# Performance work log

Measured on AMD Instinct MI355X. Metric: run time of the kernel, lower is better.

## Reference

```python
import jax, jax.numpy as jnp
import numpy as np

N, D = 100000, 128

def _seg_softmax(vals, ids, n):
    # torch scatter_reduce amax with include_self=True over zeros init => max(0, seg max);
    # softmax is shift-invariant so this matches torch exactly and stays stable.
    m = jnp.maximum(jax.ops.segment_max(vals, ids, num_segments=n), 0.0)
    e = jnp.exp(vals - m[ids])
    s = jax.ops.segment_sum(e, ids, num_segments=n)
    return e / (s[ids] + 1e-9)

def setup_inputs() -> dict:
    key = jax.random.key(0)
    ks = jax.random.split(key, 24)
    d = D
    def lin(k, fi, fo):
        b = 1.0 / np.sqrt(fi)
        kw, kb = jax.random.split(k)
        return (jax.random.uniform(kw, (fi, fo), jnp.float32, -b, b),
                jax.random.uniform(kb, (fo,), jnp.float32, -b, b))
    Wae, bae = lin(ks[0], 2 * d, d)
    w0w, w0b = lin(ks[1], d, 1)
    War, bar = lin(ks[2], 2 * d, d)
    w1w, w1b = lin(ks[3], d, 1)
    W1, b1 = lin(ks[4], d, d)
    W2, b2 = lin(ks[5], d, d)
    W3, b3 = lin(ks[6], d, d)
    return {
        'node_emb': jax.random.normal(ks[7], (N, d), jnp.float32),
        'Wae': Wae, 'bae': bae, 'w0w': w0w[:, 0], 'w0b': w0b,
        'War': War, 'bar': bar, 'w1w': w1w[:, 0], 'w1b': w1b,
        'W1': W1, 'b1': b1, 'W2': W2, 'b2': b2, 'W3': W3, 'b3': b3,
        'er_src': jax.random.randint(ks[8], (500000,), 0, N),
        'er_dst': jax.random.randint(ks[9], (500000,), 0, N),
        'ee_src': jax.random.randint(ks[10], (500000,), 0, N),
        'ee_dst': jax.random.randint(ks[11], (500000,), 0, N),
        'rr_src': jax.random.randint(ks[12], (200000,), 0, N),
        'rr_dst': jax.random.randint(ks[13], (200000,), 0, N),
    }

def reference(node_emb, Wae, bae, w0w, w0b, War, bar, w1w, w1b,
              W1, b1, W2, b2, W3, b3,
              er_src, er_dst, ee_src, ee_dst, rr_src, rr_dst):
    n = node_emb.shape[0]
    h = node_emb[er_src]              # (E, d) head entity emb
    r = node_emb[er_dst]              # (E, d) relation emb
    # entity-side attention over relation neighbours
    pair_e = jnp.concatenate([r, h], axis=-1)
    e_ij = jnp.tanh(pair_e @ Wae + bae) @ w0w + w0b[0]
    attn_e = _seg_softmax(e_ij, er_src, n)
    attn_agg = jax.ops.segment_sum(attn_e[:, None] * r, er_src, num_segments=n)
    # relation-side attention over entity neighbours (separate params)
    pair_r = jnp.concatenate([h, r], axis=-1)
    e_ij_r = jnp.tanh(pair_r @ War + bar) @ w1w + w1b[0]
    attn_r = _seg_softmax(e_ij_r, er_dst, n)
    attn_agg = attn_agg + jax.ops.segment_sum(attn_r[:, None] * h, er_dst, num_segments=n)
    # unweighted mean over similar-entity and similar-relation edges
    mean_agg = jax.ops.segment_sum(node_emb[ee_dst], ee_src, num_segments=n)
    mean_agg = mean_agg + jax.ops.segment_sum(node_emb[rr_dst], rr_src, num_segments=n)
    cnt = jax.ops.segment_sum(jnp.ones(ee_src.shape[0], node_emb.dtype), ee_src, num_segments=n)
    cnt = cnt + jax.ops.segment_sum(jnp.ones(rr_src.shape[0], node_emb.dtype), rr_src, num_segments=n)
    mean_agg = mean_agg / jnp.maximum(cnt, 1.0)[:, None]
    return (jnp.tanh(node_emb @ W1 + b1)
            + jnp.tanh(attn_agg @ W2 + b2)
            + jnp.tanh(mean_agg @ W3 + b3))
```

## Files before the change

### kernel.cpp

```cpp
#include <hip/hip_runtime.h>
#include <hip/hip_bf16.h>

#define D 128
#define TILE 2048

typedef __bf16 bf16x8 __attribute__((ext_vector_type(8)));
typedef float f32x4 __attribute__((ext_vector_type(4)));
typedef unsigned short u16x8 __attribute__((ext_vector_type(8)));

__device__ __forceinline__ float tanh_fast(float x) {
    float e = __expf(2.0f * fabsf(x));
    float t = 1.0f - 2.0f * __builtin_amdgcn_rcpf(e + 1.0f);
    return copysignf(t, x);
}

__device__ __forceinline__ float bf2f(unsigned short u) {
    return __uint_as_float((unsigned int)u << 16);
}

__device__ __forceinline__ unsigned short f2bf_u16(float x) {
    __hip_bfloat16 t = __float2bfloat16(x);
    return *(unsigned short*)&t;
}

#define SWZ_F(x, imm) __int_as_float(__builtin_amdgcn_ds_swizzle(__float_as_int(x), imm))

__global__ __launch_bounds__(256) void detect_kernel(const unsigned short* __restrict__ x,
                                                     int* __restrict__ flag) {
    int t = threadIdx.x;
    int cnt = 0;
    for (int i = t; i < 4096; i += 256) {
        unsigned e = (x[i] >> 7) & 0xFFu;
        if (e == 0xFFu || e >= 0x90u || (e >= 1u && e <= 0x6Eu)) cnt++;
    }
    __shared__ int sh[256];
    sh[t] = cnt;
    __syncthreads();
    for (int off = 128; off; off >>= 1) {
        if (t < off) sh[t] += sh[t + off];
        __syncthreads();
    }
    if (t == 0) flag[0] = (sh[0] > 800) ? 1 : 0;
}

struct ConvBatch {
    const void* src[14];
    __hip_bfloat16* dst[14];
    int n[14];
};

__global__ __launch_bounds__(256) void conv_weights_kernel(ConvBatch cb,
                                                           const int* __restrict__ flag) {
    int a = blockIdx.y;
    const void* s = cb.src[a];
    unsigned short* d = (unsigned short*)cb.dst[a];
    int n = cb.n[a];
    int f = flag[0];
    int i = (blockIdx.x * 256 + threadIdx.x) * 4;
    if (i >= n) return;
    if (i + 4 <= n) {
        ushort4 o;
        if (f) {
            float4 v = *(const float4*)((const float*)s + i);
            o.x = f2bf_u16(v.x); o.y = f2bf_u16(v.y);
            o.z = f2bf_u16(v.z); o.w = f2bf_u16(v.w);
        } else {
            o = *(const ushort4*)((const unsigned short*)s + i);
        }
        *(ushort4*)(d + i) = o;
    } else {
        for (int j = i; j < n; j++)
            d[j] = f ? f2bf_u16(((const float*)s)[j])
                     : ((const unsigned short*)s)[j];
    }
}

__global__ __launch_bounds__(256) void conv_x_kernel(const void* __restrict__ src,
                                                     __hip_bfloat16* __restrict__ dst,
                                                     int n, const int* __restrict__ flag) {
    int i = (blockIdx.x * 256 + threadIdx.x) * 4;
    if (i >= n) return;
    int f = flag[0];
    ushort4 o;
    if (f) {
        float4 v = *(const float4*)((const float*)src + i);
        o.x = f2bf_u16(v.x); o.y = f2bf_u16(v.y);
        o.z = f2bf_u16(v.z); o.w = f2bf_u16(v.w);
    } else {
        o = *(const ushort4*)((const unsigned short*)src + i);
    }
    *(ushort4*)((unsigned short*)dst + i) = o;
}

struct TransBatch {
    const void* base[7];
    int off[7];
    unsigned short* dst[7];
};

__global__ __launch_bounds__(256) void trans_kernel(TransBatch tb,
                                                    const int* __restrict__ flag) {
    int a = blockIdx.y;
    int f = flag[0];
    const float* sf = (const float*)tb.base[a] + tb.off[a];
    const unsigned short* sb = (const unsigned short*)tb.base[a] + tb.off[a];
    unsigned short* d = tb.dst[a];
    int idx = (blockIdx.x * 256 + threadIdx.x) * 4;
    int k = idx >> 7, c = idx & 127;
    unsigned short v[4];
    if (f) {
        float4 x = *(const float4*)(sf + idx);
        v[0] = f2bf_u16(x.x); v[1] = f2bf_u16(x.y);
        v[2] = f2bf_u16(x.z); v[3] = f2bf_u16(x.w);
    } else {
        ushort4 x = *(const ushort4*)(sb + idx);
        v[0] = x.x; v[1] = x.y; v[2] = x.z; v[3] = x.w;
    }
#pragma unroll
    for (int j = 0; j < 4; j++) d[(c + j) * 128 + k] = v[j];
}

__global__ __launch_bounds__(256) void zero_kernel(int* p, int n) {
    int i = blockIdx.x * 256 + threadIdx.x;
    if (i < n) p[i] = 0;
}

__global__ __launch_bounds__(256) void count_kernel(const int* __restrict__ keys, int E,
                                                    int* __restrict__ deg) {
    int i = blockIdx.x * 256 + threadIdx.x;
    if (i < E) atomicAdd(&deg[keys[i]], 1);
}

__global__ __launch_bounds__(256) void scan_partial_kernel(const int* __restrict__ deg,
                                                           int* __restrict__ tsum,
                                                           int N, int ntpa) {
    int a = blockIdx.x / ntpa, t = blockIdx.x % ntpa;
    const int* d = deg + (size_t)a * N + (size_t)t * TILE;
    int lim = N - t * TILE; if (lim > TILE) lim = TILE;
    int base = threadIdx.x * 8;
    int s = 0;
#pragma unroll
    for (int j = 0; j < 8; j++) {
        int i = base + j;
        if (i < lim) s += d[i];
    }
    __shared__ int sh[256];
    sh[threadIdx.x] = s;
    __syncthreads();
    for (int off = 128; off; off >>= 1) {
        if (threadIdx.x < off) sh[threadIdx.x] += sh[threadIdx.x + off];
        __syncthreads();
    }
    if (threadIdx.x == 0) tsum[blockIdx.x] = sh[0];
}

__global__ __launch_bounds__(256) void scan_tiles_kernel(const int* __restrict__ tsum,
                                                         int* __restrict__ toff,
                                                         int* __restrict__ indptr,
                                                         int N, int ntpa) {
    __shared__ int tmp[256];
    int t = threadIdx.x;
    for (int a = 0; a < 4; a++) {
        int v = (t < ntpa) ? tsum[a * ntpa + t] : 0;
        tmp[t] = v;
        __syncthreads();
        for (int off = 1; off < 256; off <<= 1) {
            int u = (t >= off) ? tmp[t - off] : 0;
            __syncthreads();
            tmp[t] += u;
            __syncthreads();
        }
        if (t < ntpa) toff[a * ntpa + t] = tmp[t] - v;
        if (t == ntpa - 1) indptr[(size_t)a * (N + 1) + N] = tmp[t];
        __syncthreads();
    }
}

__global__ __launch_bounds__(256) void scan_final_kernel(int* __restrict__ degcur,
                                                         const int* __restrict__ toff,
                                                         int* __restrict__ indptr,
                                                         int N, int ntpa) {
    int a = blockIdx.x / ntpa, t = blockIdx.x % ntpa;
    int* d = degcur + (size_t)a * N + (size_t)t * TILE;
    int* ip = indptr + (size_t)a * (N + 1) + (size_t)t * TILE;
    int lim = N - t * TILE; if (lim > TILE) lim = TILE;
    int base = threadIdx.x * 8;
    int v[8];
    int s = 0;
#pragma unroll
    for (int j = 0; j < 8; j++) {
        int i = base + j;
        v[j] = (i < lim) ? d[i] : 0;
        s += v[j];
    }
    __shared__ int tmp[256];
    tmp[threadIdx.x] = s;
    __syncthreads();
    for (int off = 1; off < 256; off <<= 1) {
        int u = (threadIdx.x >= off) ? tmp[threadIdx.x - off] : 0;
        __syncthreads();
        tmp[threadIdx.x] += u;
        __syncthreads();
    }
    int run = toff[blockIdx.x] + tmp[threadIdx.x] - s;
#pragma unroll
    for (int j = 0; j < 8; j++) {
        int i = base + j;
        if (i < lim) { ip[i] = run; d[i] = run; run += v[j]; }
    }
}

__global__ __launch_bounds__(256) void scatter_attn_kernel(const int* __restrict__ keys,
                                                           const int* __restrict__ oths, int E,
                                                           int* __restrict__ cursor,
                                                           int* __restrict__ key_sorted,
                                                           int* __restrict__ oth_sorted) {
    int i = blockIdx.x * 256 + threadIdx.x;
    if (i < E) {
        int k = keys[i];
        int p = atomicAdd(&cursor[k], 1);
        key_sorted[p] = k;
        oth_sorted[p] = oths[i];
    }
}

__global__ __launch_bounds__(256) void scatter_mean_kernel(const int* __restrict__ keys,
                                                           const int* __restrict__ dsts, int E,
                                                           int* __restrict__ cursor,
                                                           int* __restrict__ dst_sorted) {
    int i = blockIdx.x * 256 + threadIdx.x;
    if (i < E) {
        int p = atomicAdd(&cursor[keys[i]], 1);
        dst_sorted[p] = dsts[i];
    }
}

__global__ __launch_bounds__(256) void gemm2_mfma_kernel(
    const __hip_bfloat16* __restrict__ X,
    const unsigned short* __restrict__ Wt,
    const __hip_bfloat16* __restrict__ bias,
    __hip_bfloat16* __restrict__ part0,
    __hip_bfloat16* __restrict__ part1, int N) {
    __shared__ __align__(16) unsigned short As[64 * 136];
    __shared__ __align__(16) unsigned short Bs[128 * 136];
    int n0 = blockIdx.x * 64;
    for (int idx = threadIdx.x; idx < 64 * 16; idx += 256) {
        int r = idx >> 4, ch = idx & 15;
        uint4 v = make_uint4(0u, 0u, 0u, 0u);
        int n = n0 + r;
        if (n < N) v = ((const uint4*)(X + (size_t)n * D))[ch];
        *(uint4*)&As[r * 136 + ch * 8] = v;
    }
    int w = threadIdx.x >> 6, lane = threadIdx.x & 63;
    int n15 = lane & 15, quad = lane >> 4;
    bf16x8 af[4];
    for (int half = 0; half < 2; half++) {
        for (int idx = threadIdx.x; idx < 128 * 16; idx += 256) {
            int r = idx >> 4, ch = idx & 15;
            uint4 v = ((const uint4*)(Wt + (size_t)(half * 128 + r) * D))[ch];
            *(uint4*)&Bs[r * 136 + ch * 8] = v;
        }
        __syncthreads();
        if (half == 0) {
            const unsigned short* arow = &As[(w * 16 + n15) * 136 + quad * 8];
#pragma unroll
            for (int t = 0; t < 4; t++) af[t] = *(const bf16x8*)(arow + t * 32);
        }
        __hip_bfloat16* outp = half ? part1 : part0;
        for (int c = 0; c < 8; c++) {
            f32x4 acc = {0.f, 0.f, 0.f, 0.f};
            const unsigned short* brow = &Bs[(c * 16 + n15) * 136 + quad * 8];
#pragma unroll
            for (int t = 0; t < 4; t++)
                acc = __builtin_amdgcn_mfma_f32_16x16x32_bf16(
                    af[t], *(const bf16x8*)(brow + t * 32), acc, 0, 0, 0);
            int col = c * 16 + n15;
            float b = half ? __bfloat162float(bias[col]) : 0.f;
#pragma unroll
            for (int i = 0; i < 4; i++) {
                int row = n0 + w * 16 + quad * 4 + i;
                if (row < N) outp[(size_t)row * D + col] = __float2bfloat16(acc[i] + b);
            }
        }
        if (half == 0) __syncthreads();
    }
}

__global__ __launch_bounds__(256) void final_mfma_kernel(
    const __hip_bfloat16* __restrict__ X, const __hip_bfloat16* __restrict__ Agg,
    const __hip_bfloat16* __restrict__ Mn,
    const unsigned short* __restrict__ Wt1, const __hip_bfloat16* __restrict__ b1,
    const unsigned short* __restrict__ Wt2, const __hip_bfloat16* __restrict__ b2,
    const unsigned short* __restrict__ Wt3, const __hip_bfloat16* __restrict__ b3,
    void* __restrict__ out, const int* __restrict__ flag, int N) {
    __shared__ __align__(16) unsigned short As[64 * 136];
    __shared__ __align__(16) unsigned short Bs[128 * 136];
    int n0 = blockIdx.x * 64;
    int w = threadIdx.x >> 6, lane = threadIdx.x & 63;
    int n15 = lane & 15, quad = lane >> 4;
    float osum[8][4];
#pragma unroll
    for (int c = 0; c < 8; c++)
#pragma unroll
        for (int i = 0; i < 4; i++) osum[c][i] = 0.f;
    const __hip_bfloat16* srcs[3] = {X, Agg, Mn};
    const unsigned short* Wts[3] = {Wt1, Wt2, Wt3};
    const __hip_bfloat16* bs[3] = {b1, b2, b3};
    for (int m = 0; m < 3; m++) {
        if (m > 0) __syncthreads();
        const __hip_bfloat16* S = srcs[m];
        const unsigned short* Wm = Wts[m];
        for (int idx = threadIdx.x; idx < 64 * 16; idx += 256) {
            int r = idx >> 4, ch = idx & 15;
            uint4 v = make_uint4(0u, 0u, 0u, 0u);
            int n = n0 + r;
            if (n < N) v = ((const uint4*)(S + (size_t)n * D))[ch];
            *(uint4*)&As[r * 136 + ch * 8] = v;
        }
        for (int idx = threadIdx.x; idx < 128 * 16; idx += 256) {
            int r = idx >> 4, ch = idx & 15;
            uint4 v = ((const uint4*)(Wm + (size_t)r * D))[ch];
            *(uint4*)&Bs[r * 136 + ch * 8] = v;
        }
        __syncthreads();
        const unsigned short* arow = &As[(w * 16 + n15) * 136 + quad * 8];
        bf16x8 af[4];
#pragma unroll
        for (int t = 0; t < 4; t++) af[t] = *(const bf16x8*)(arow + t * 32);
        for (int c = 0; c < 8; c++) {
            f32x4 acc = {0.f, 0.f, 0.f, 0.f};
            const unsigned short* brow = &Bs[(c * 16 + n15) * 136 + quad * 8];
#pragma unroll
            for (int t = 0; t < 4; t++)
                acc = __builtin_amdgcn_mfma_f32_16x16x32_bf16(
                    af[t], *(const bf16x8*)(brow + t * 32), acc, 0, 0, 0);
            float bb = __bfloat162float(bs[m][c * 16 + n15]);
#pragma unroll
            for (int i = 0; i < 4; i++) osum[c][i] += tanh_fast(acc[i] + bb);
        }
    }
    int f = flag[0];
    for (int c = 0; c < 8; c++) {
        int col = c * 16 + n15;
#pragma unroll
        for (int i = 0; i < 4; i++) {
            int row = n0 + w * 16 + quad * 4 + i;
            if (row < N) {
                if (f) ((float*)out)[(size_t)row * D + col] = osum[c][i];
                else   ((__hip_bfloat16*)out)[(size_t)row * D + col] =
                           __float2bfloat16(osum[c][i]);
            }
        }
    }
}

__global__ __launch_bounds__(256) void edge_score_kernel(
    const __hip_bfloat16* __restrict__ Pkey,
    const __hip_bfloat16* __restrict__ Poth,
    const int* __restrict__ key_s,
    const int* __restrict__ oth_s,
    const __hip_bfloat16* __restrict__ w,
    const __hip_bfloat16* __restrict__ wb,
    float* __restrict__ eij, int E) {
    int l = threadIdx.x & 15;
    int gid = (int)((blockIdx.x * 256 + threadIdx.x) >> 4);
    int ngroups = (int)((gridDim.x * 256) >> 4);
    u16x8 wv = *(const u16x8*)((const unsigned short*)w + l * 8);
    float wf[8];
#pragma unroll
    for (int j = 0; j < 8; j++) wf[j] = bf2f(wv[j]);
    float wbv = bf2f(*(const unsigned short*)wb);
    const unsigned short* PK = (const unsigned short*)Pkey;
    const unsigned short* PO = (const unsigned short*)Poth;
    for (int s = gid; s < E; s += ngroups) {
        int key = key_s[s], oth = oth_s[s];
        u16x8 a = *(const u16x8*)(PK + (size_t)key * D + l * 8);
        u16x8 b = *(const u16x8*)(PO + (size_t)oth * D + l * 8);
        float p = 0.f;
#pragma unroll
        for (int j = 0; j < 8; j++)
            p = fmaf(tanh_fast(bf2f(a[j]) + bf2f(b[j])), wf[j], p);
        p += SWZ_F(p, 0x041F);
        p += SWZ_F(p, 0x081F);
        p += SWZ_F(p, 0x101F);
        p += SWZ_F(p, 0x201F);
        if (l == 0) eij[s] = p + wbv;
    }
}

__global__ __launch_bounds__(256) void attn_node_kernel(
    const __hip_bfloat16* __restrict__ X,
    const float* __restrict__ eij_e, const int* __restrict__ ip_e,
    const int* __restrict__ oth_e,
    const float* __restrict__ eij_r, const int* __restrict__ ip_r,
    const int* __restrict__ oth_r,
    __hip_bfloat16* __restrict__ attn_agg, int N) {
    int g = (int)((blockIdx.x * 256 + threadIdx.x) >> 4);
    int l = threadIdx.x & 15;
    if (g >= N) return;
    const unsigned short* Xp = (const unsigned short*)X;
    float acc[8];
#pragma unroll
    for (int j = 0; j < 8; j++) acc[j] = 0.f;
    for (int side = 0; side < 2; side++) {
        const float* eij = side ? eij_r : eij_e;
        const int* ip  = side ? ip_r  : ip_e;
        const int* oth = side ? oth_r : oth_e;
        int s0 = ip[g], s1 = ip[g + 1];
        if (s1 == s0) continue;
        float m = 0.f;
        for (int i = s0 + l; i < s1; i += 16) m = fmaxf(m, eij[i]);
        m = fmaxf(m, SWZ_F(m, 0x041F));
        m = fmaxf(m, SWZ_F(m, 0x081F));
        m = fmaxf(m, SWZ_F(m, 0x101F));
        m = fmaxf(m, SWZ_F(m, 0x201F));
        float ssum = 0.f;
        for (int i = s0 + l; i < s1; i += 16) ssum += __expf(eij[i] - m);
        ssum += SWZ_F(ssum, 0x041F);
        ssum += SWZ_F(ssum, 0x081F);
        ssum += SWZ_F(ssum, 0x101F);
        ssum += SWZ_F(ssum, 0x201F);
        float inv = 1.f / (ssum + 1e-9f);
        int i = s0;
        for (; i + 2 <= s1; i += 2) {
            int o0 = oth[i], o1 = oth[i + 1];
            u16x8 x0 = *(const u16x8*)(Xp + (size_t)o0 * D + l * 8);
            u16x8 x1 = *(const u16x8*)(Xp + (size_t)o1 * D + l * 8);
            float p0 = __expf(eij[i] - m) * inv;
            float p1 = __expf(eij[i + 1] - m) * inv;
#pragma unroll
            for (int j = 0; j < 8; j++)
                acc[j] += p0 * bf2f(x0[j]) + p1 * bf2f(x1[j]);
        }
        if (i < s1) {
            int o0 = oth[i];
            u16x8 x0 = *(const u16x8*)(Xp + (size_t)o0 * D + l * 8);
            float p0 = __expf(eij[i] - m) * inv;
#pragma unroll
            for (int j = 0; j < 8; j++) acc[j] += p0 * bf2f(x0[j]);
        }
    }
    u16x8 ov;
#pragma unroll
    for (int j = 0; j < 8; j++) ov[j] = f2bf_u16(acc[j]);
    *(u16x8*)((unsigned short*)attn_agg + (size_t)g * D + l * 8) = ov;
}

__global__ __launch_bounds__(256) void mean_node_kernel(
    const __hip_bfloat16* __restrict__ X,
    const int* __restrict__ ip_ee, const int* __restrict__ dst_ee,
    const int* __restrict__ ip_rr, const int* __restrict__ dst_rr,
    __hip_bfloat16* __restrict__ mean_agg, int N) {
    int g = (int)((blockIdx.x * 256 + threadIdx.x) >> 4);
    int l = threadIdx.x & 15;
    if (g >= N) return;
    const unsigned short* Xp = (const unsigned short*)X;
    float acc[8];
#pragma unroll
    for (int j = 0; j < 8; j++) acc[j] = 0.f;
    int cnt = 0;
    for (int side = 0; side < 2; side++) {
        const int* ip  = side ? ip_rr  : ip_ee;
        const int* dst = side ? dst_rr : dst_ee;
        int s0 = ip[g], s1 = ip[g + 1];
        cnt += s1 - s0;
        int i = s0;
        for (; i + 2 <= s1; i += 2) {
            int o0 = dst[i], o1 = dst[i + 1];
            u16x8 x0 = *(const u16x8*)(Xp + (size_t)o0 * D + l * 8);
            u16x8 x1 = *(const u16x8*)(Xp + (size_t)o1 * D + l * 8);
#pragma unroll
            for (int j = 0; j < 8; j++)
                acc[j] += bf2f(x0[j]) + bf2f(x1[j]);
        }
        if (i < s1) {
            u16x8 x0 = *(const u16x8*)(Xp + (size_t)dst[i] * D + l * 8);
#pragma unroll
            for (int j = 0; j < 8; j++) acc[j] += bf2f(x0[j]);
        }
    }
    float inv = 1.f / fmaxf((float)cnt, 1.f);
    u16x8 ov;
#pragma unroll
    for (int j = 0; j < 8; j++) ov[j] = f2bf_u16(acc[j] * inv);
    *(u16x8*)((unsigned short*)mean_agg + (size_t)g * D + l * 8) = ov;
}

extern "C" void kernel_launch(void* const* d_in, const int* in_sizes, int n_in,
                              void* d_out, int out_size, void* d_ws, size_t ws_size,
                              hipStream_t stream) {
    const int* er_src = (const int*)d_in[15];
    const int* er_dst = (const int*)d_in[16];
    const int* ee_src = (const int*)d_in[17];
    const int* ee_dst = (const int*)d_in[18];
    const int* rr_src = (const int*)d_in[19];
    const int* rr_dst = (const int*)d_in[20];

    int N   = in_sizes[0] / D;
    int Eer = in_sizes[15];
    int Eee = in_sizes[17];
    int Err = in_sizes[19];

    char* ws = (char*)d_ws;
    size_t off = 0;
    auto alloc = [&](size_t bytes) -> void* {
        void* p = ws + off;
        off = (off + bytes + 255) & ~(size_t)255;
        return p;
    };
    int ntpa = (N + TILE - 1) / TILE;
    int T = 4 * ntpa;
    int* flag   = (int*)alloc(256);
    int* key_se = (int*)alloc((size_t)Eer * 4);
    int* key_sr = (int*)alloc((size_t)Eer * 4);
    int* oth_e  = (int*)alloc((size_t)Eer * 4);
    int* oth_r  = (int*)alloc((size_t)Eer * 4);
    int* dst_ee = (int*)alloc((size_t)Eee * 4);
    int* dst_rr = (int*)alloc((size_t)Err * 4);
    int* indptr = (int*)alloc((size_t)4 * (N + 1) * 4);
    int* degcur = (int*)alloc((size_t)4 * N * 4);
    int* tsum   = (int*)alloc((size_t)T * 4);
    int* toff   = (int*)alloc((size_t)T * 4);
    float* eij_e = (float*)alloc((size_t)Eer * 4);
    float* eij_r = (float*)alloc((size_t)Eer * 4);
    __hip_bfloat16* Xc = (__hip_bfloat16*)alloc((size_t)N * D * 2);
    __hip_bfloat16* part0 = (__hip_bfloat16*)alloc((size_t)N * D * 2);
    __hip_bfloat16* part1 = (__hip_bfloat16*)alloc((size_t)N * D * 2);
    __hip_bfloat16* attn_agg = part0;
    __hip_bfloat16* mean_agg = part1;
    unsigned short* WtA = (unsigned short*)alloc((size_t)256 * 128 * 2);
    unsigned short* WtR = (unsigned short*)alloc((size_t)256 * 128 * 2);
    unsigned short* Wt1 = (unsigned short*)alloc((size_t)128 * 128 * 2);
    unsigned short* Wt2 = (unsigned short*)alloc((size_t)128 * 128 * 2);
    unsigned short* Wt3 = (unsigned short*)alloc((size_t)128 * 128 * 2);
    ConvBatch cb;
    int widx[14] = {1, 2, 3, 4, 5, 6, 7, 8, 9, 10, 11, 12, 13, 14};
    for (int i = 0; i < 14; i++) {
        cb.src[i] = d_in[widx[i]];
        cb.n[i] = in_sizes[widx[i]];
        cb.dst[i] = (__hip_bfloat16*)alloc((size_t)cb.n[i] * 2);
    }
    const __hip_bfloat16* bae = cb.dst[1];
    const __hip_bfloat16* w0w = cb.dst[2];
    const __hip_bfloat16* w0b = cb.dst[3];
    const __hip_bfloat16* bar_= cb.dst[5];
    const __hip_bfloat16* w1w = cb.dst[6];
    const __hip_bfloat16* w1b = cb.dst[7];
    const __hip_bfloat16* b1  = cb.dst[9];
    const __hip_bfloat16* b2  = cb.dst[11];
    const __hip_bfloat16* b3  = cb.dst[13];
    (void)n_in; (void)out_size;
    if (off > ws_size) return;

    detect_kernel<<<1, 256, 0, stream>>>((const unsigned short*)d_in[0], flag);
    conv_weights_kernel<<<dim3(32, 14), 256, 0, stream>>>(cb, flag);
    conv_x_kernel<<<(N * D / 4 + 255) / 256, 256, 0, stream>>>(d_in[0], Xc, N * D, flag);
    TransBatch tb;
    tb.base[0] = d_in[1];  tb.off[0] = 0;         tb.dst[0] = WtA;
    tb.base[1] = d_in[1];  tb.off[1] = 128 * 128; tb.dst[1] = WtA + 128 * 128;
    tb.base[2] = d_in[5];  tb.off[2] = 0;         tb.dst[2] = WtR;
    tb.base[3] = d_in[5];  tb.off[3] = 128 * 128; tb.dst[3] = WtR + 128 * 128;
    tb.base[4] = d_in[9];  tb.off[4] = 0;         tb.dst[4] = Wt1;
    tb.base[5] = d_in[11]; tb.off[5] = 0;         tb.dst[5] = Wt2;
    tb.base[6] = d_in[13]; tb.off[6] = 0;         tb.dst[6] = Wt3;
    trans_kernel<<<dim3(16, 7), 256, 0, stream>>>(tb, flag);

    zero_kernel<<<(4 * N + 255) / 256, 256, 0, stream>>>(degcur, 4 * N);
    count_kernel<<<(Eer + 255) / 256, 256, 0, stream>>>(er_src, Eer, degcur);
    count_kernel<<<(Eer + 255) / 256, 256, 0, stream>>>(er_dst, Eer, degcur + N);
    count_kernel<<<(Eee + 255) / 256, 256, 0, stream>>>(ee_src, Eee, degcur + 2 * N);
    count_kernel<<<(Err + 255) / 256, 256, 0, stream>>>(rr_src, Err, degcur + 3 * N);
    scan_partial_kernel<<<T, 256, 0, stream>>>(degcur, tsum, N, ntpa);
    scan_tiles_kernel<<<1, 256, 0, stream>>>(tsum, toff, indptr, N, ntpa);
    scan_final_kernel<<<T, 256, 0, stream>>>(degcur, toff, indptr, N, ntpa);
    scatter_attn_kernel<<<(Eer + 255) / 256, 256, 0, stream>>>(er_src, er_dst, Eer,
                                                               degcur, key_se, oth_e);
    scatter_attn_kernel<<<(Eer + 255) / 256, 256, 0, stream>>>(er_dst, er_src, Eer,
                                                               degcur + N, key_sr, oth_r);
    scatter_mean_kernel<<<(Eee + 255) / 256, 256, 0, stream>>>(ee_src, ee_dst, Eee,
                                                               degcur + 2 * N, dst_ee);
    scatter_mean_kernel<<<(Err + 255) / 256, 256, 0, stream>>>(rr_src, rr_dst, Err,
                                                               degcur + 3 * N, dst_rr);

    int GB = (N + 63) / 64;
    int EB = 2048;

    gemm2_mfma_kernel<<<GB, 256, 0, stream>>>(Xc, WtA, bae, part0, part1, N);
    edge_score_kernel<<<EB, 256, 0, stream>>>(part1, part0, key_se, oth_e,
                                              w0w, w0b, eij_e, Eer);

    gemm2_mfma_kernel<<<GB, 256, 0, stream>>>(Xc, WtR, bar_, part0, part1, N);
    edge_score_kernel<<<EB, 256, 0, stream>>>(part1, part0, key_sr, oth_r,
                                              w1w, w1b, eij_r, Eer);

    int NG = (N + 15) / 16;
    attn_node_kernel<<<NG, 256, 0, stream>>>(Xc, eij_e, indptr, oth_e,
                                             eij_r, indptr + (N + 1), oth_r,
                                             attn_agg, N);
    mean_node_kernel<<<NG, 256, 0, stream>>>(Xc, indptr + 2 * (N + 1), dst_ee,
                                             indptr + 3 * (N + 1), dst_rr,
                                             mean_agg, N);
    final_mfma_kernel<<<GB, 256, 0, stream>>>(Xc, attn_agg, mean_agg,
                                              Wt1, b1, Wt2, b2, Wt3, b3,
                                              d_out, flag, N);
}
```

Before: 583.8 us.

## Keep GEMM weights resident in LDS and load activations directly to registers

The gemm2 and final MFMA kernels now load all weight matrices into shared memory once per block. They then loop over row tiles in a grid-stride fashion, reading activation fragments straight from global memory into registers instead of staging them through LDS. Block sizes grow to 512 and 1024 threads, and the grids are capped at 2048 blocks. This removes the repeated weight reloads and per-tile barriers, but the larger LDS footprint (about 104 KB in the final kernel) can limit occupancy.

```diff
diff --git a/kernel.cpp b/kernel.cpp
--- a/kernel.cpp
+++ b/kernel.cpp
@@ -235,120 +235,126 @@
     }
 }
 
-__global__ __launch_bounds__(256) void gemm2_mfma_kernel(
+__global__ __launch_bounds__(512) void gemm2_mfma_kernel(
     const __hip_bfloat16* __restrict__ X,
     const unsigned short* __restrict__ Wt,
     const __hip_bfloat16* __restrict__ bias,
     __hip_bfloat16* __restrict__ part0,
     __hip_bfloat16* __restrict__ part1, int N) {
-    __shared__ __align__(16) unsigned short As[64 * 136];
-    __shared__ __align__(16) unsigned short Bs[128 * 136];
-    int n0 = blockIdx.x * 64;
-    for (int idx = threadIdx.x; idx < 64 * 16; idx += 256) {
+    __shared__ __align__(16) unsigned short Bs[256 * 136];
+    for (int idx = threadIdx.x; idx < 256 * 16; idx += 512) {
         int r = idx >> 4, ch = idx & 15;
-        uint4 v = make_uint4(0u, 0u, 0u, 0u);
-        int n = n0 + r;
-        if (n < N) v = ((const uint4*)(X + (size_t)n * D))[ch];
-        *(uint4*)&As[r * 136 + ch * 8] = v;
-    }
+        *(uint4*)&Bs[r * 136 + ch * 8] = ((const uint4*)(Wt + (size_t)r * D))[ch];
+    }
+    __syncthreads();
     int w = threadIdx.x >> 6, lane = threadIdx.x & 63;
     int n15 = lane & 15, quad = lane >> 4;
-    bf16x8 af[4];
-    for (int half = 0; half < 2; half++) {
-        for (int idx = threadIdx.x; idx < 128 * 16; idx += 256) {
-            int r = idx >> 4, ch = idx & 15;
-            uint4 v = ((const uint4*)(Wt + (size_t)(half * 128 + r) * D))[ch];
-            *(uint4*)&Bs[r * 136 + ch * 8] = v;
-        }
-        __syncthreads();
-        if (half == 0) {
-            const unsigned short* arow = &As[(w * 16 + n15) * 136 + quad * 8];
-#pragma unroll
-            for (int t = 0; t < 4; t++) af[t] = *(const bf16x8*)(arow + t * 32);
-        }
-        __hip_bfloat16* outp = half ? part1 : part0;
-        for (int c = 0; c < 8; c++) {
-            f32x4 acc = {0.f, 0.f, 0.f, 0.f};
-            const unsigned short* brow = &Bs[(c * 16 + n15) * 136 + quad * 8];
-#pragma unroll
-            for (int t = 0; t < 4; t++)
-                acc = __builtin_amdgcn_mfma_f32_16x16x32_bf16(
-                    af[t], *(const bf16x8*)(brow + t * 32), acc, 0, 0, 0);
-            int col = c * 16 + n15;
-            float b = half ? __bfloat162float(bias[col]) : 0.f;
-#pragma unroll
-            for (int i = 0; i < 4; i++) {
-                int row = n0 + w * 16 + quad * 4 + i;
-                if (row < N) outp[(size_t)row * D + col] = __float2bfloat16(acc[i] + b);
+    float bv[8];
+#pragma unroll
+    for (int c = 0; c < 8; c++) bv[c] = __bfloat162float(bias[c * 16 + n15]);
+    int ntiles = (N + 127) >> 7;
+    for (int tile = blockIdx.x; tile < ntiles; tile += gridDim.x) {
+        int r0 = tile * 128 + w * 16;
+        int arow = r0 + n15;
+        const unsigned short* ap = (const unsigned short*)X + (size_t)arow * D + quad * 8;
+        bf16x8 af[4];
+#pragma unroll
+        for (int t = 0; t < 4; t++) {
+            bf16x8 v = {};
+            if (arow < N) v = *(const bf16x8*)(ap + t * 32);
+            af[t] = v;
+        }
+#pragma unroll
+        for (int half = 0; half < 2; half++) {
+            __hip_bfloat16* outp = half ? part1 : part0;
+            for (int c = 0; c < 8; c++) {
+                f32x4 acc = {0.f, 0.f, 0.f, 0.f};
+                const unsigned short* brow = &Bs[(half * 128 + c * 16 + n15) * 136 + quad * 8];
+#pragma unroll
+                for (int t = 0; t < 4; t++)
+                    acc = __builtin_amdgcn_mfma_f32_16x16x32_bf16(
+                        af[t], *(const bf16x8*)(brow + t * 32), acc, 0, 0, 0);
+                int col = c * 16 + n15;
+                float b = half ? bv[c] : 0.f;
+#pragma unroll
+                for (int i = 0; i < 4; i++) {
+                    int row = r0 + quad * 4 + i;
+                    if (row < N) outp[(size_t)row * D + col] = __float2bfloat16(acc[i] + b);
+                }
             }
         }
-        if (half == 0) __syncthreads();
-    }
-}
-
-__global__ __launch_bounds__(256) void final_mfma_kernel(
+    }
+}
+
+__global__ __launch_bounds__(1024) void final_mfma_kernel(
     const __hip_bfloat16* __restrict__ X, const __hip_bfloat16* __restrict__ Agg,
     const __hip_bfloat16* __restrict__ Mn,
     const unsigned short* __restrict__ Wt1, const __hip_bfloat16* __restrict__ b1,
     const unsigned short* __restrict__ Wt2, const __hip_bfloat16* __restrict__ b2,
     const unsigned short* __restrict__ Wt3, const __hip_bfloat16* __restrict__ b3,
     void* __restrict__ out, const int* __restrict__ flag, int N) {
-    __shared__ __align__(16) unsigned short As[64 * 136];
-    __shared__ __align__(16) unsigned short Bs[128 * 136];
-    int n0 = blockIdx.x * 64;
+    __shared__ __align__(16) unsigned short Bs[3 * 128 * 136];
+#pragma unroll
+    for (int m = 0; m < 3; m++) {
+        const unsigned short* Wm = (m == 0) ? Wt1 : (m == 1) ? Wt2 : Wt3;
+        for (int idx = threadIdx.x; idx < 128 * 16; idx += 1024) {
+            int r = idx >> 4, ch = idx & 15;
+            *(uint4*)&Bs[(m * 128 + r) * 136 + ch * 8] =
+                ((const uint4*)(Wm + (size_t)r * D))[ch];
+        }
+    }
+    __syncthreads();
     int w = threadIdx.x >> 6, lane = threadIdx.x & 63;
     int n15 = lane & 15, quad = lane >> 4;
-    float osum[8][4];
-#pragma unroll
-    for (int c = 0; c < 8; c++)
-#pragma unroll
-        for (int i = 0; i < 4; i++) osum[c][i] = 0.f;
-    const __hip_bfloat16* srcs[3] = {X, Agg, Mn};
-    const unsigned short* Wts[3] = {Wt1, Wt2, Wt3};
-    const __hip_bfloat16* bs[3] = {b1, b2, b3};
+    float bv[3][8];
+#pragma unroll
     for (int m = 0; m < 3; m++) {
-        if (m > 0) __syncthreads();
-        const __hip_bfloat16* S = srcs[m];
-        const unsigned short* Wm = Wts[m];
-        for (int idx = threadIdx.x; idx < 64 * 16; idx += 256) {
-            int r = idx >> 4, ch = idx & 15;
-            uint4 v = make_uint4(0u, 0u, 0u, 0u);
-            int n = n0 + r;
-            if (n < N) v = ((const uint4*)(S + (size_t)n * D))[ch];
-            *(uint4*)&As[r * 136 + ch * 8] = v;
-        }
-        for (int idx = threadIdx.x; idx < 128 * 16; idx += 256) {
-            int r = idx >> 4, ch = idx & 15;
-            uint4 v = ((const uint4*)(Wm + (size_t)r * D))[ch];
-            *(uint4*)&Bs[r * 136 + ch * 8] = v;
-        }
-        __syncthreads();
-        const unsigned short* arow = &As[(w * 16 + n15) * 136 + quad * 8];
-        bf16x8 af[4];
-#pragma unroll
-        for (int t = 0; t < 4; t++) af[t] = *(const bf16x8*)(arow + t * 32);
+        const __hip_bfloat16* bm = (m == 0) ? b1 : (m == 1) ? b2 : b3;
+#pragma unroll
+        for (int c = 0; c < 8; c++) bv[m][c] = __bfloat162float(bm[c * 16 + n15]);
+    }
+    int f = flag[0];
+    int ntiles = (N + 255) >> 8;
+    for (int tile = blockIdx.x; tile < ntiles; tile += gridDim.x) {
+        int r0 = tile * 256 + w * 16;
+        int arow = r0 + n15;
+        float osum[8][4];
+#pragma unroll
+        for (int c = 0; c < 8; c++)
+#pragma unroll
+            for (int i = 0; i < 4; i++) osum[c][i] = 0.f;
+#pragma unroll
+        for (int m = 0; m < 3; m++) {
+            const __hip_bfloat16* S = (m == 0) ? X : (m == 1) ? Agg : Mn;
+            const unsigned short* ap = (const unsigned short*)S + (size_t)arow * D + quad * 8;
+            bf16x8 af[4];
+#pragma unroll
+            for (int t = 0; t < 4; t++) {
+                bf16x8 v = {};
+                if (arow < N) v = *(const bf16x8*)(ap + t * 32);
+                af[t] = v;
+            }
+            for (int c = 0; c < 8; c++) {
+                f32x4 acc = {0.f, 0.f, 0.f, 0.f};
+                const unsigned short* brow = &Bs[(m * 128 + c * 16 + n15) * 136 + quad * 8];
+#pragma unroll
+                for (int t = 0; t < 4; t++)
+                    acc = __builtin_amdgcn_mfma_f32_16x16x32_bf16(
+                        af[t], *(const bf16x8*)(brow + t * 32), acc, 0, 0, 0);
+#pragma unroll
+                for (int i = 0; i < 4; i++) osum[c][i] += tanh_fast(acc[i] + bv[m][c]);
+            }
+        }
         for (int c = 0; c < 8; c++) {
-            f32x4 acc = {0.f, 0.f, 0.f, 0.f};
-            const unsigned short* brow = &Bs[(c * 16 + n15) * 136 + quad * 8];
-#pragma unroll
-            for (int t = 0; t < 4; t++)
-                acc = __builtin_amdgcn_mfma_f32_16x16x32_bf16(
-                    af[t], *(const bf16x8*)(brow + t * 32), acc, 0, 0, 0);
-            float bb = __bfloat162float(bs[m][c * 16 + n15]);
-#pragma unroll
-            for (int i = 0; i < 4; i++) osum[c][i] += tanh_fast(acc[i] + bb);
-        }
-    }
-    int f = flag[0];
-    for (int c = 0; c < 8; c++) {
-        int col = c * 16 + n15;
-#pragma unroll
-        for (int i = 0; i < 4; i++) {
-            int row = n0 + w * 16 + quad * 4 + i;
-            if (row < N) {
-                if (f) ((float*)out)[(size_t)row * D + col] = osum[c][i];
-                else   ((__hip_bfloat16*)out)[(size_t)row * D + col] =
-                           __float2bfloat16(osum[c][i]);
+            int col = c * 16 + n15;
+#pragma unroll
+            for (int i = 0; i < 4; i++) {
+                int row = r0 + quad * 4 + i;
+                if (row < N) {
+                    if (f) ((float*)out)[(size_t)row * D + col] = osum[c][i];
+                    else   ((__hip_bfloat16*)out)[(size_t)row * D + col] =
+                               __float2bfloat16(osum[c][i]);
+                }
             }
         }
     }
@@ -582,14 +588,17 @@
     scatter_mean_kernel<<<(Err + 255) / 256, 256, 0, stream>>>(rr_src, rr_dst, Err,
                                                                degcur + 3 * N, dst_rr);
 
-    int GB = (N + 63) / 64;
+    int nt128 = (N + 127) / 128;
+    int G2 = nt128 < 2048 ? nt128 : 2048;
+    int nt256 = (N + 255) / 256;
+    int GF = nt256 < 2048 ? nt256 : 2048;
     int EB = 2048;
 
-    gemm2_mfma_kernel<<<GB, 256, 0, stream>>>(Xc, WtA, bae, part0, part1, N);
+    gemm2_mfma_kernel<<<G2, 512, 0, stream>>>(Xc, WtA, bae, part0, part1, N);
     edge_score_kernel<<<EB, 256, 0, stream>>>(part1, part0, key_se, oth_e,
                                               w0w, w0b, eij_e, Eer);
 
-    gemm2_mfma_kernel<<<GB, 256, 0, stream>>>(Xc, WtR, bar_, part0, part1, N);
+    gemm2_mfma_kernel<<<G2, 512, 0, stream>>>(Xc, WtR, bar_, part0, part1, N);
     edge_score_kernel<<<EB, 256, 0, stream>>>(part1, part0, key_sr, oth_r,
                                               w1w, w1b, eij_r, Eer);
 
@@ -600,7 +609,7 @@
     mean_node_kernel<<<NG, 256, 0, stream>>>(Xc, indptr + 2 * (N + 1), dst_ee,
                                              indptr + 3 * (N + 1), dst_rr,
                                              mean_agg, N);
-    final_mfma_kernel<<<GB, 256, 0, stream>>>(Xc, attn_agg, mean_agg,
-                                              Wt1, b1, Wt2, b2, Wt3, b3,
-                                              d_out, flag, N);
-}
+    final_mfma_kernel<<<GF, 1024, 0, stream>>>(Xc, attn_agg, mean_agg,
+                                               Wt1, b1, Wt2, b2, Wt3, b3,
+                                               d_out, flag, N);
+}
```

Result: slower. 1.007 ms (+72.4%).
